# Optimization experiments

Hardware: AMD Instinct MI355X
Metric: run time of the kernel (lower is better)

## Reference

```python
import jax, jax.numpy as jnp
import numpy as np

B, T, D, H = 256, 1024, 64, 128


def _orthogonal(key, shape):
    a = jax.random.normal(key, (max(shape), max(shape)), dtype=jnp.float32)
    q, _ = jnp.linalg.qr(a)
    return q[: shape[0], : shape[1]].astype(jnp.float32)


def setup_inputs() -> dict:
    key = jax.random.key(0)
    k0, k1, k2, k3 = jax.random.split(key, 4)
    x = jax.random.normal(k0, (B, T, D), dtype=jnp.float32)
    W_xK = _orthogonal(k1, (H, D))
    W_xz = _orthogonal(k2, (H, D))
    W_hK = _orthogonal(k3, (H, H))
    b_xK = jnp.zeros((H,), jnp.float32)
    b_xz = jnp.zeros((H,), jnp.float32)
    b_hK = jnp.zeros((H,), jnp.float32)
    return {"x": x, "W_xK": W_xK, "b_xK": b_xK, "W_xz": W_xz,
            "b_xz": b_xz, "W_hK": W_hK, "b_hK": b_hK}


def reference(x, W_xK, b_xK, W_xz, b_xz, W_hK, b_hK):
    # Precompute input projections for all timesteps (batched GEMM).
    gate_x_K = jnp.einsum('btd,hd->bth', x, W_xK) + b_xK  # [B,T,H]
    gate_x_z = jnp.einsum('btd,hd->bth', x, W_xz) + b_xz  # [B,T,H]
    z_all = jnp.tanh(gate_x_z)                             # [B,T,H]
    h0 = jnp.zeros((x.shape[0], W_hK.shape[0]), x.dtype)

    def step(h, inputs):
        gxK, z = inputs  # each [B,H]
        gate_h_K = h @ W_hK.T + b_hK
        K_gain = jax.nn.sigmoid(gxK + gate_h_K)
        h_new = jnp.tanh(h + K_gain * (z - h))
        return h_new, h_new

    # scan over time dim
    _, outs = jax.lax.scan(step, h0,
                           (jnp.swapaxes(gate_x_K, 0, 1),
                            jnp.swapaxes(z_all, 0, 1)))
    outs = jnp.swapaxes(outs, 0, 1)  # [B,T,H]
    return (outs, outs)
```

## Files before the change

kernel.cpp:

```cpp
#include <hip/hip_runtime.h>
#include <hip/hip_fp16.h>

#define NB 256
#define NT 1024
#define ND 64
#define NH 128

typedef __fp16 half8 __attribute__((ext_vector_type(8)));
typedef __fp16 half4v __attribute__((ext_vector_type(4)));
typedef float float4v __attribute__((ext_vector_type(4)));

static __device__ __forceinline__ float fast_tanh(float v) {
    float e = __expf(2.0f * v);
    return 1.0f - 2.0f * __builtin_amdgcn_rcpf(e + 1.0f);
}

static __device__ __forceinline__ void fast_barrier() {
    asm volatile("s_waitcnt lgkmcnt(0)\n\ts_barrier" ::: "memory");
}

__global__ __launch_bounds__(512, 1) void fused_rnn_v8(
        const float* __restrict__ x,
        const float* __restrict__ WxK, const float* __restrict__ bxK,
        const float* __restrict__ Wxz, const float* __restrict__ bxz,
        const float* __restrict__ Whk, const float* __restrict__ bhk,
        float* __restrict__ out) {
    __shared__ __align__(16) __fp16 hbuf[2][128];
    __shared__ __align__(16) __fp16 gT[2][128][24];
    __shared__ __align__(16) __fp16 zT[2][128][24];

    const int tid = threadIdx.x;
    const int b = blockIdx.x;
    const int w = tid >> 6, lane = tid & 63;
    const int l16 = lane & 15, kg = lane >> 4;
    const int j = w * 16 + l16;

    half8 whT[4];
    #pragma unroll
    for (int kt = 0; kt < 4; ++kt) {
        const float* p = Whk + (size_t)j * NH + kt * 32 + kg * 8;
        float4v u = *(const float4v*)p, v = *(const float4v*)(p + 4);
        whT[kt] = (half8){(__fp16)u.x, (__fp16)u.y, (__fp16)u.z, (__fp16)u.w,
                          (__fp16)v.x, (__fp16)v.y, (__fp16)v.z, (__fp16)v.w};
    }

    half8 wxT[2][2];
    #pragma unroll
    for (int mat = 0; mat < 2; ++mat) {
        const float* W = mat ? Wxz : WxK;
        #pragma unroll
        for (int kt = 0; kt < 2; ++kt) {
            const float* p = W + (size_t)j * ND + kt * 32 + kg * 8;
            float4v u = *(const float4v*)p, v = *(const float4v*)(p + 4);
            wxT[mat][kt] = (half8){(__fp16)u.x, (__fp16)u.y, (__fp16)u.z, (__fp16)u.w,
                                   (__fp16)v.x, (__fp16)v.y, (__fp16)v.z, (__fp16)v.w};
        }
    }
    const float bGK = bxK[j] + bhk[j];
    const float bZ  = bxz[j];
    const float4v zero4 = {0.f, 0.f, 0.f, 0.f};

    const float* xb = x + (size_t)b * NT * ND;
    float4v xf[4];

    auto xload = [&](int c) {
        const float* px = xb + (size_t)c * 16 * 64 + (size_t)l16 * 64;
        #pragma unroll
        for (int kt = 0; kt < 2; ++kt) {
            const float* qp = px + kt * 32 + kg * 8;
            xf[2 * kt]     = *(const float4v*)qp;
            xf[2 * kt + 1] = *(const float4v*)(qp + 4);
        }
    };

    auto proj = [&](int dst) {
        half8 ax[2];
        #pragma unroll
        for (int kt = 0; kt < 2; ++kt) {
            float4v u = xf[2 * kt], v = xf[2 * kt + 1];
            ax[kt] = (half8){(__fp16)u.x, (__fp16)u.y, (__fp16)u.z, (__fp16)u.w,
                             (__fp16)v.x, (__fp16)v.y, (__fp16)v.z, (__fp16)v.w};
        }
        float4v pg = __builtin_amdgcn_mfma_f32_16x16x32_f16(ax[0], wxT[0][0], zero4, 0, 0, 0);
        pg = __builtin_amdgcn_mfma_f32_16x16x32_f16(ax[1], wxT[0][1], pg, 0, 0, 0);
        half4v hg = {(__fp16)(pg[0] + bGK), (__fp16)(pg[1] + bGK),
                     (__fp16)(pg[2] + bGK), (__fp16)(pg[3] + bGK)};
        *(half4v*)&gT[dst][j][kg * 4] = hg;
        float4v pz = __builtin_amdgcn_mfma_f32_16x16x32_f16(ax[0], wxT[1][0], zero4, 0, 0, 0);
        pz = __builtin_amdgcn_mfma_f32_16x16x32_f16(ax[1], wxT[1][1], pz, 0, 0, 0);
        half4v hz = {(__fp16)fast_tanh(pz[0] + bZ), (__fp16)fast_tanh(pz[1] + bZ),
                     (__fp16)fast_tanh(pz[2] + bZ), (__fp16)fast_tanh(pz[3] + bZ)};
        *(half4v*)&zT[dst][j][kg * 4] = hz;
    };

    xload(0);
    if (tid < 128) hbuf[0][tid] = (__fp16)0.0f;
    proj(0);
    xload(1);
    __syncthreads();

    float hn = 0.0f;
    float oreg[16];
    const size_t CPY = (size_t)NB * NT * NH;
    float* obase = out + (size_t)b * NT * NH + (kg == 1 ? CPY : 0);

    for (int c = 0; c < 64; ++c) {
        const int cb = c & 1;

        half8 gA = *(const half8*)&gT[cb][j][0];
        half8 gB = *(const half8*)&gT[cb][j][8];
        half8 zA = *(const half8*)&zT[cb][j][0];
        half8 zB = *(const half8*)&zT[cb][j][8];

        #pragma unroll
        for (int s = 0; s < 16; ++s) {
            const int p = s & 1;
            half8 ah0 = *(const half8*)&hbuf[p][0 * 32 + kg * 8];
            half8 ah1 = *(const half8*)&hbuf[p][1 * 32 + kg * 8];
            half8 ah2 = *(const half8*)&hbuf[p][2 * 32 + kg * 8];
            half8 ah3 = *(const half8*)&hbuf[p][3 * 32 + kg * 8];

            const float gv = (float)(s < 8 ? gA[s & 7] : gB[s & 7]);
            const float zv = (float)(s < 8 ? zA[s & 7] : zB[s & 7]);
            const float d = zv - hn;

            float4v aA = __builtin_amdgcn_mfma_f32_16x16x32_f16(ah0, whT[0], zero4, 0, 0, 0);
            float4v aB = __builtin_amdgcn_mfma_f32_16x16x32_f16(ah2, whT[2], zero4, 0, 0, 0);
            aA = __builtin_amdgcn_mfma_f32_16x16x32_f16(ah1, whT[1], aA, 0, 0, 0);
            aB = __builtin_amdgcn_mfma_f32_16x16x32_f16(ah3, whT[3], aB, 0, 0, 0);
            const float y = aA[0] + aB[0];

            const float K = __builtin_amdgcn_rcpf(1.0f + __expf(-(y + gv)));
            hn = fast_tanh(__builtin_fmaf(K, d, hn));
            oreg[s] = hn;

            if (kg == 0) hbuf[p ^ 1][j] = (__fp16)hn;
            fast_barrier();
        }

        if (kg < 2) {
            float* po = obase + (size_t)(c * 16) * NH;
            #pragma unroll
            for (int s = 0; s < 16; ++s) {
                po[j] = oreg[s];
                po += NH;
            }
        }

        if (c < 63) {
            proj(cb ^ 1);
            if (c < 62) xload(c + 2);
        }
    }
}

extern "C" void kernel_launch(void* const* d_in, const int* in_sizes, int n_in,
                              void* d_out, int out_size, void* d_ws, size_t ws_size,
                              hipStream_t stream) {
    (void)in_sizes; (void)n_in; (void)d_ws; (void)ws_size; (void)out_size;
    const float* x   = (const float*)d_in[0];
    const float* WxK = (const float*)d_in[1];
    const float* bxK = (const float*)d_in[2];
    const float* Wxz = (const float*)d_in[3];
    const float* bxz = (const float*)d_in[4];
    const float* Whk = (const float*)d_in[5];
    const float* bhk = (const float*)d_in[6];
    float* out = (float*)d_out;

    fused_rnn_v8<<<256, 512, 0, stream>>>(x, WxK, bxK, Wxz, bxz, Whk, bhk, out);
}
```

Before: 502.5 us.

## Interleave next-chunk input projection into recurrent steps and shorten per-step latency

Moves the next chunk's input projection (MFMAs, bias, tanh, LDS stores) and the x prefetch out of the gap between chunks and spreads them across specific timesteps inside the serial recurrence. The aim is to hide that work in the barrier-bound latency of each step. The step itself changes too: the four recurrent MFMAs become independent accumulations summed at the end, and the gate and z values are pre-converted to float, with the sigmoid's scale folded in, once per chunk. Exp2-based tanh and sigmoid replace the expf versions, and launch bounds now request 2 blocks per CU, which may limit registers. The extra live registers and the work placed inside steps could lengthen the critical path.

```diff
diff --git a/kernel.cpp b/kernel.cpp
--- a/kernel.cpp
+++ b/kernel.cpp
@@ -10,16 +10,27 @@
 typedef __fp16 half4v __attribute__((ext_vector_type(4)));
 typedef float float4v __attribute__((ext_vector_type(4)));
 
-static __device__ __forceinline__ float fast_tanh(float v) {
-    float e = __expf(2.0f * v);
-    return 1.0f - 2.0f * __builtin_amdgcn_rcpf(e + 1.0f);
+#define LOG2E 1.44269504f
+#define TWO_LOG2E 2.88539008f
+
+static __device__ __forceinline__ float exp2_fast(float x) {
+#if __has_builtin(__builtin_amdgcn_exp2f)
+    return __builtin_amdgcn_exp2f(x);
+#else
+    return __expf(x * 0.69314718f);
+#endif
+}
+
+static __device__ __forceinline__ float ftanh(float v) {
+    float t = __builtin_amdgcn_rcpf(exp2_fast(v * TWO_LOG2E) + 1.0f);
+    return __builtin_fmaf(-2.0f, t, 1.0f);
 }
 
 static __device__ __forceinline__ void fast_barrier() {
     asm volatile("s_waitcnt lgkmcnt(0)\n\ts_barrier" ::: "memory");
 }
 
-__global__ __launch_bounds__(512, 1) void fused_rnn_v8(
+__global__ __launch_bounds__(512, 2) void fused_rnn_v9(
         const float* __restrict__ x,
         const float* __restrict__ WxK, const float* __restrict__ bxK,
         const float* __restrict__ Wxz, const float* __restrict__ bxz,
@@ -88,8 +99,8 @@
         *(half4v*)&gT[dst][j][kg * 4] = hg;
         float4v pz = __builtin_amdgcn_mfma_f32_16x16x32_f16(ax[0], wxT[1][0], zero4, 0, 0, 0);
         pz = __builtin_amdgcn_mfma_f32_16x16x32_f16(ax[1], wxT[1][1], pz, 0, 0, 0);
-        half4v hz = {(__fp16)fast_tanh(pz[0] + bZ), (__fp16)fast_tanh(pz[1] + bZ),
-                     (__fp16)fast_tanh(pz[2] + bZ), (__fp16)fast_tanh(pz[3] + bZ)};
+        half4v hz = {(__fp16)ftanh(pz[0] + bZ), (__fp16)ftanh(pz[1] + bZ),
+                     (__fp16)ftanh(pz[2] + bZ), (__fp16)ftanh(pz[3] + bZ)};
         *(half4v*)&zT[dst][j][kg * 4] = hz;
     };
 
@@ -111,6 +122,17 @@
         half8 gB = *(const half8*)&gT[cb][j][8];
         half8 zA = *(const half8*)&zT[cb][j][0];
         half8 zB = *(const half8*)&zT[cb][j][8];
+        float glf[16], zvf[16];
+        #pragma unroll
+        for (int i = 0; i < 8; ++i) {
+            glf[i]     = -(float)gA[i] * LOG2E;
+            glf[i + 8] = -(float)gB[i] * LOG2E;
+            zvf[i]     = (float)zA[i];
+            zvf[i + 8] = (float)zB[i];
+        }
+
+        half8 ax0, ax1;
+        float4v pg, pz;
 
         #pragma unroll
         for (int s = 0; s < 16; ++s) {
@@ -120,21 +142,46 @@
             half8 ah2 = *(const half8*)&hbuf[p][2 * 32 + kg * 8];
             half8 ah3 = *(const half8*)&hbuf[p][3 * 32 + kg * 8];
 
-            const float gv = (float)(s < 8 ? gA[s & 7] : gB[s & 7]);
-            const float zv = (float)(s < 8 ? zA[s & 7] : zB[s & 7]);
-            const float d = zv - hn;
+            const float d = zvf[s] - hn;
 
             float4v aA = __builtin_amdgcn_mfma_f32_16x16x32_f16(ah0, whT[0], zero4, 0, 0, 0);
-            float4v aB = __builtin_amdgcn_mfma_f32_16x16x32_f16(ah2, whT[2], zero4, 0, 0, 0);
-            aA = __builtin_amdgcn_mfma_f32_16x16x32_f16(ah1, whT[1], aA, 0, 0, 0);
-            aB = __builtin_amdgcn_mfma_f32_16x16x32_f16(ah3, whT[3], aB, 0, 0, 0);
-            const float y = aA[0] + aB[0];
-
-            const float K = __builtin_amdgcn_rcpf(1.0f + __expf(-(y + gv)));
-            hn = fast_tanh(__builtin_fmaf(K, d, hn));
+            float4v aB = __builtin_amdgcn_mfma_f32_16x16x32_f16(ah1, whT[1], zero4, 0, 0, 0);
+            float4v aC = __builtin_amdgcn_mfma_f32_16x16x32_f16(ah2, whT[2], zero4, 0, 0, 0);
+            float4v aD = __builtin_amdgcn_mfma_f32_16x16x32_f16(ah3, whT[3], zero4, 0, 0, 0);
+            const float y = (aA[0] + aB[0]) + (aC[0] + aD[0]);
+
+            const float K = __builtin_amdgcn_rcpf(
+                1.0f + exp2_fast(__builtin_fmaf(y, -LOG2E, glf[s])));
+            hn = ftanh(__builtin_fmaf(K, d, hn));
             oreg[s] = hn;
 
             if (kg == 0) hbuf[p ^ 1][j] = (__fp16)hn;
+
+            if (s == 1 && c < 63) {
+                float4v u0 = xf[0], v0 = xf[1], u1 = xf[2], v1 = xf[3];
+                ax0 = (half8){(__fp16)u0.x, (__fp16)u0.y, (__fp16)u0.z, (__fp16)u0.w,
+                              (__fp16)v0.x, (__fp16)v0.y, (__fp16)v0.z, (__fp16)v0.w};
+                ax1 = (half8){(__fp16)u1.x, (__fp16)u1.y, (__fp16)u1.z, (__fp16)u1.w,
+                              (__fp16)v1.x, (__fp16)v1.y, (__fp16)v1.z, (__fp16)v1.w};
+                pg = __builtin_amdgcn_mfma_f32_16x16x32_f16(ax0, wxT[0][0], zero4, 0, 0, 0);
+                pg = __builtin_amdgcn_mfma_f32_16x16x32_f16(ax1, wxT[0][1], pg, 0, 0, 0);
+            }
+            if (s == 3 && c < 63) {
+                pz = __builtin_amdgcn_mfma_f32_16x16x32_f16(ax0, wxT[1][0], zero4, 0, 0, 0);
+                pz = __builtin_amdgcn_mfma_f32_16x16x32_f16(ax1, wxT[1][1], pz, 0, 0, 0);
+            }
+            if (s == 5 && c < 63) {
+                half4v hg = {(__fp16)(pg[0] + bGK), (__fp16)(pg[1] + bGK),
+                             (__fp16)(pg[2] + bGK), (__fp16)(pg[3] + bGK)};
+                *(half4v*)&gT[cb ^ 1][j][kg * 4] = hg;
+            }
+            if (s == 7 && c < 63) {
+                half4v hz = {(__fp16)ftanh(pz[0] + bZ), (__fp16)ftanh(pz[1] + bZ),
+                             (__fp16)ftanh(pz[2] + bZ), (__fp16)ftanh(pz[3] + bZ)};
+                *(half4v*)&zT[cb ^ 1][j][kg * 4] = hz;
+            }
+            if (s == 9 && c < 62) xload(c + 2);
+
             fast_barrier();
         }
 
@@ -145,11 +192,6 @@
                 po[j] = oreg[s];
                 po += NH;
             }
-        }
-
-        if (c < 63) {
-            proj(cb ^ 1);
-            if (c < 62) xload(c + 2);
         }
     }
 }
@@ -167,5 +209,5 @@
     const float* bhk = (const float*)d_in[6];
     float* out = (float*)d_out;
 
-    fused_rnn_v8<<<256, 512, 0, stream>>>(x, WxK, bxK, Wxz, bxz, Whk, bhk, out);
-}
+    fused_rnn_v9<<<256, 512, 0, stream>>>(x, WxK, bxK, Wxz, bxz, Whk, bhk, out);
+}
```

New measurement: 542.6 us. +8.0%, slower.

## Process two batch sequences per block to interleave independent recurrences

Applied to the files above, without the earlier changes.

Each workgroup now runs two independent batch rows at once, interleaving their MFMA chains and nonlinearities within each timestep. The two sequences share a single barrier per step, so the latency-bound serial chain gets independent work to hide MFMA and transcendental latency. The grid halves to 128 blocks, which leaves about half of the MI355X's CUs idle. Register pressure and LDS use also roughly double, and the launch bounds now ask for two blocks per CU.

```diff
diff --git a/kernel.cpp b/kernel.cpp
--- a/kernel.cpp
+++ b/kernel.cpp
@@ -19,18 +19,18 @@
     asm volatile("s_waitcnt lgkmcnt(0)\n\ts_barrier" ::: "memory");
 }
 
-__global__ __launch_bounds__(512, 1) void fused_rnn_v8(
+__global__ __launch_bounds__(512, 2) void fused_rnn_v10(
         const float* __restrict__ x,
         const float* __restrict__ WxK, const float* __restrict__ bxK,
         const float* __restrict__ Wxz, const float* __restrict__ bxz,
         const float* __restrict__ Whk, const float* __restrict__ bhk,
         float* __restrict__ out) {
-    __shared__ __align__(16) __fp16 hbuf[2][128];
-    __shared__ __align__(16) __fp16 gT[2][128][24];
-    __shared__ __align__(16) __fp16 zT[2][128][24];
+    __shared__ __align__(16) __fp16 hbufA[2][128], hbufB[2][128];
+    __shared__ __align__(16) __fp16 gTA[2][128][24], gTB[2][128][24];
+    __shared__ __align__(16) __fp16 zTA[2][128][24], zTB[2][128][24];
 
     const int tid = threadIdx.x;
-    const int b = blockIdx.x;
+    const int b0 = blockIdx.x * 2, b1 = b0 + 1;
     const int w = tid >> 6, lane = tid & 63;
     const int l16 = lane & 15, kg = lane >> 4;
     const int j = w * 16 + l16;
@@ -43,7 +43,6 @@
         whT[kt] = (half8){(__fp16)u.x, (__fp16)u.y, (__fp16)u.z, (__fp16)u.w,
                           (__fp16)v.x, (__fp16)v.y, (__fp16)v.z, (__fp16)v.w};
     }
-
     half8 wxT[2][2];
     #pragma unroll
     for (int mat = 0; mat < 2; ++mat) {
@@ -60,10 +59,11 @@
     const float bZ  = bxz[j];
     const float4v zero4 = {0.f, 0.f, 0.f, 0.f};
 
-    const float* xb = x + (size_t)b * NT * ND;
-    float4v xf[4];
-
-    auto xload = [&](int c) {
+    const float* xbA = x + (size_t)b0 * NT * ND;
+    const float* xbB = x + (size_t)b1 * NT * ND;
+    float4v xfA[4], xfB[4];
+
+    auto xload = [&](const float* xb, float4v (&xf)[4], int c) {
         const float* px = xb + (size_t)c * 16 * 64 + (size_t)l16 * 64;
         #pragma unroll
         for (int kt = 0; kt < 2; ++kt) {
@@ -73,83 +73,112 @@
         }
     };
 
-    auto proj = [&](int dst) {
-        half8 ax[2];
-        #pragma unroll
-        for (int kt = 0; kt < 2; ++kt) {
-            float4v u = xf[2 * kt], v = xf[2 * kt + 1];
-            ax[kt] = (half8){(__fp16)u.x, (__fp16)u.y, (__fp16)u.z, (__fp16)u.w,
-                             (__fp16)v.x, (__fp16)v.y, (__fp16)v.z, (__fp16)v.w};
-        }
-        float4v pg = __builtin_amdgcn_mfma_f32_16x16x32_f16(ax[0], wxT[0][0], zero4, 0, 0, 0);
-        pg = __builtin_amdgcn_mfma_f32_16x16x32_f16(ax[1], wxT[0][1], pg, 0, 0, 0);
+    auto proj = [&](float4v (&xf)[4], __fp16 (*gT)[128][24], __fp16 (*zT)[128][24], int dst) {
+        half8 ax0, ax1;
+        {
+            float4v u0 = xf[0], v0 = xf[1], u1 = xf[2], v1 = xf[3];
+            ax0 = (half8){(__fp16)u0.x, (__fp16)u0.y, (__fp16)u0.z, (__fp16)u0.w,
+                          (__fp16)v0.x, (__fp16)v0.y, (__fp16)v0.z, (__fp16)v0.w};
+            ax1 = (half8){(__fp16)u1.x, (__fp16)u1.y, (__fp16)u1.z, (__fp16)u1.w,
+                          (__fp16)v1.x, (__fp16)v1.y, (__fp16)v1.z, (__fp16)v1.w};
+        }
+        float4v pg = __builtin_amdgcn_mfma_f32_16x16x32_f16(ax0, wxT[0][0], zero4, 0, 0, 0);
+        pg = __builtin_amdgcn_mfma_f32_16x16x32_f16(ax1, wxT[0][1], pg, 0, 0, 0);
         half4v hg = {(__fp16)(pg[0] + bGK), (__fp16)(pg[1] + bGK),
                      (__fp16)(pg[2] + bGK), (__fp16)(pg[3] + bGK)};
         *(half4v*)&gT[dst][j][kg * 4] = hg;
-        float4v pz = __builtin_amdgcn_mfma_f32_16x16x32_f16(ax[0], wxT[1][0], zero4, 0, 0, 0);
-        pz = __builtin_amdgcn_mfma_f32_16x16x32_f16(ax[1], wxT[1][1], pz, 0, 0, 0);
+        float4v pz = __builtin_amdgcn_mfma_f32_16x16x32_f16(ax0, wxT[1][0], zero4, 0, 0, 0);
+        pz = __builtin_amdgcn_mfma_f32_16x16x32_f16(ax1, wxT[1][1], pz, 0, 0, 0);
         half4v hz = {(__fp16)fast_tanh(pz[0] + bZ), (__fp16)fast_tanh(pz[1] + bZ),
                      (__fp16)fast_tanh(pz[2] + bZ), (__fp16)fast_tanh(pz[3] + bZ)};
         *(half4v*)&zT[dst][j][kg * 4] = hz;
     };
 
-    xload(0);
-    if (tid < 128) hbuf[0][tid] = (__fp16)0.0f;
-    proj(0);
-    xload(1);
+    xload(xbA, xfA, 0);
+    xload(xbB, xfB, 0);
+    if (tid < 128) {
+        hbufA[0][tid] = (__fp16)0.0f;
+        hbufB[0][tid] = (__fp16)0.0f;
+    }
+    proj(xfA, gTA, zTA, 0);
+    proj(xfB, gTB, zTB, 0);
+    xload(xbA, xfA, 1);
+    xload(xbB, xfB, 1);
     __syncthreads();
 
-    float hn = 0.0f;
-    float oreg[16];
+    float hnA = 0.0f, hnB = 0.0f;
+    float oregA[16], oregB[16];
     const size_t CPY = (size_t)NB * NT * NH;
-    float* obase = out + (size_t)b * NT * NH + (kg == 1 ? CPY : 0);
+    float* obase = out + (size_t)(kg < 2 ? b0 : b1) * NT * NH
+                 + ((kg & 1) ? CPY : 0) + j;
 
     for (int c = 0; c < 64; ++c) {
         const int cb = c & 1;
 
-        half8 gA = *(const half8*)&gT[cb][j][0];
-        half8 gB = *(const half8*)&gT[cb][j][8];
-        half8 zA = *(const half8*)&zT[cb][j][0];
-        half8 zB = *(const half8*)&zT[cb][j][8];
+        half8 gAa = *(const half8*)&gTA[cb][j][0], gAb = *(const half8*)&gTA[cb][j][8];
+        half8 zAa = *(const half8*)&zTA[cb][j][0], zAb = *(const half8*)&zTA[cb][j][8];
+        half8 gBa = *(const half8*)&gTB[cb][j][0], gBb = *(const half8*)&gTB[cb][j][8];
+        half8 zBa = *(const half8*)&zTB[cb][j][0], zBb = *(const half8*)&zTB[cb][j][8];
 
         #pragma unroll
         for (int s = 0; s < 16; ++s) {
             const int p = s & 1;
-            half8 ah0 = *(const half8*)&hbuf[p][0 * 32 + kg * 8];
-            half8 ah1 = *(const half8*)&hbuf[p][1 * 32 + kg * 8];
-            half8 ah2 = *(const half8*)&hbuf[p][2 * 32 + kg * 8];
-            half8 ah3 = *(const half8*)&hbuf[p][3 * 32 + kg * 8];
-
-            const float gv = (float)(s < 8 ? gA[s & 7] : gB[s & 7]);
-            const float zv = (float)(s < 8 ? zA[s & 7] : zB[s & 7]);
-            const float d = zv - hn;
-
-            float4v aA = __builtin_amdgcn_mfma_f32_16x16x32_f16(ah0, whT[0], zero4, 0, 0, 0);
-            float4v aB = __builtin_amdgcn_mfma_f32_16x16x32_f16(ah2, whT[2], zero4, 0, 0, 0);
-            aA = __builtin_amdgcn_mfma_f32_16x16x32_f16(ah1, whT[1], aA, 0, 0, 0);
-            aB = __builtin_amdgcn_mfma_f32_16x16x32_f16(ah3, whT[3], aB, 0, 0, 0);
-            const float y = aA[0] + aB[0];
-
-            const float K = __builtin_amdgcn_rcpf(1.0f + __expf(-(y + gv)));
-            hn = fast_tanh(__builtin_fmaf(K, d, hn));
-            oreg[s] = hn;
-
-            if (kg == 0) hbuf[p ^ 1][j] = (__fp16)hn;
+            half8 aA0 = *(const half8*)&hbufA[p][0 * 32 + kg * 8];
+            half8 aA1 = *(const half8*)&hbufA[p][1 * 32 + kg * 8];
+            half8 aA2 = *(const half8*)&hbufA[p][2 * 32 + kg * 8];
+            half8 aA3 = *(const half8*)&hbufA[p][3 * 32 + kg * 8];
+            half8 aB0 = *(const half8*)&hbufB[p][0 * 32 + kg * 8];
+            half8 aB1 = *(const half8*)&hbufB[p][1 * 32 + kg * 8];
+            half8 aB2 = *(const half8*)&hbufB[p][2 * 32 + kg * 8];
+            half8 aB3 = *(const half8*)&hbufB[p][3 * 32 + kg * 8];
+
+            const float gvA = (float)(s < 8 ? gAa[s & 7] : gAb[s & 7]);
+            const float zvA = (float)(s < 8 ? zAa[s & 7] : zAb[s & 7]);
+            const float gvB = (float)(s < 8 ? gBa[s & 7] : gBb[s & 7]);
+            const float zvB = (float)(s < 8 ? zBa[s & 7] : zBb[s & 7]);
+            const float dA = zvA - hnA;
+            const float dB = zvB - hnB;
+
+            float4v mA0 = __builtin_amdgcn_mfma_f32_16x16x32_f16(aA0, whT[0], zero4, 0, 0, 0);
+            float4v mA1 = __builtin_amdgcn_mfma_f32_16x16x32_f16(aA2, whT[2], zero4, 0, 0, 0);
+            float4v mB0 = __builtin_amdgcn_mfma_f32_16x16x32_f16(aB0, whT[0], zero4, 0, 0, 0);
+            float4v mB1 = __builtin_amdgcn_mfma_f32_16x16x32_f16(aB2, whT[2], zero4, 0, 0, 0);
+            mA0 = __builtin_amdgcn_mfma_f32_16x16x32_f16(aA1, whT[1], mA0, 0, 0, 0);
+            mA1 = __builtin_amdgcn_mfma_f32_16x16x32_f16(aA3, whT[3], mA1, 0, 0, 0);
+            mB0 = __builtin_amdgcn_mfma_f32_16x16x32_f16(aB1, whT[1], mB0, 0, 0, 0);
+            mB1 = __builtin_amdgcn_mfma_f32_16x16x32_f16(aB3, whT[3], mB1, 0, 0, 0);
+
+            const float yA = mA0[0] + mA1[0];
+            const float yB = mB0[0] + mB1[0];
+
+            const float KA = __builtin_amdgcn_rcpf(1.0f + __expf(-(yA + gvA)));
+            const float KB = __builtin_amdgcn_rcpf(1.0f + __expf(-(yB + gvB)));
+            hnA = fast_tanh(__builtin_fmaf(KA, dA, hnA));
+            hnB = fast_tanh(__builtin_fmaf(KB, dB, hnB));
+            oregA[s] = hnA;
+            oregB[s] = hnB;
+
+            if (kg == 0) hbufA[p ^ 1][j] = (__fp16)hnA;
+            if (kg == 1) hbufB[p ^ 1][j] = (__fp16)hnB;
             fast_barrier();
         }
 
-        if (kg < 2) {
+        {
             float* po = obase + (size_t)(c * 16) * NH;
             #pragma unroll
             for (int s = 0; s < 16; ++s) {
-                po[j] = oreg[s];
+                *po = (kg < 2) ? oregA[s] : oregB[s];
                 po += NH;
             }
         }
 
         if (c < 63) {
-            proj(cb ^ 1);
-            if (c < 62) xload(c + 2);
+            proj(xfA, gTA, zTA, cb ^ 1);
+            proj(xfB, gTB, zTB, cb ^ 1);
+            if (c < 62) {
+                xload(xbA, xfA, c + 2);
+                xload(xbB, xfB, c + 2);
+            }
         }
     }
 }
@@ -167,5 +196,5 @@
     const float* bhk = (const float*)d_in[6];
     float* out = (float*)d_out;
 
-    fused_rnn_v8<<<256, 512, 0, stream>>>(x, WxK, bxK, Wxz, bxz, Whk, bhk, out);
-}
+    fused_rnn_v10<<<128, 512, 0, stream>>>(x, WxK, bxK, Wxz, bxz, Whk, bhk, out);
+}
```

Result: slower. 707.4 us (+40.8%).
